# Performance work log

Hardware: AMD Instinct MI355X
Metric: run time of the kernel (lower is better)

Reference implementation:

```python
import jax, jax.numpy as jnp
import numpy as np

B, S, E, H = 32, 4096, 1024, 16
D = E // H  # head_dim = 64


def setup_inputs() -> dict:
    key = jax.random.key(0)
    ks = jax.random.split(key, 6)
    scale = 1.0 / np.sqrt(E)
    x = jax.random.normal(ks[0], (B, S, E), dtype=jnp.float32)
    mask = jax.random.randint(ks[1], (B, S), 0, 2).astype(bool)  # True = masked key
    in_proj_w = jax.random.uniform(ks[2], (3 * E, E), jnp.float32, -scale, scale)
    in_proj_b = jnp.zeros((3 * E,), jnp.float32)
    out_w = jax.random.uniform(ks[3], (E, E), jnp.float32, -scale, scale)
    out_b = jnp.zeros((E,), jnp.float32)
    return {"x": x, "mask": mask, "in_proj_w": in_proj_w, "in_proj_b": in_proj_b,
            "out_w": out_w, "out_b": out_b}


def reference(x, mask, in_proj_w, in_proj_b, out_w, out_b):
    # nn.MultiheadAttention with q = x[:, 0:1, :], k = v = x, key_padding_mask=mask
    Wq, Wk, Wv = in_proj_w[:E], in_proj_w[E:2 * E], in_proj_w[2 * E:]
    bq, bk, bv = in_proj_b[:E], in_proj_b[E:2 * E], in_proj_b[2 * E:]
    q = (x[:, 0, :] @ Wq.T + bq).reshape(B, H, D)            # (B,H,D)
    k = (x @ Wk.T + bk).reshape(B, S, H, D)                  # (B,S,H,D)
    v = (x @ Wv.T + bv).reshape(B, S, H, D)
    scores = jnp.einsum('bhd,bshd->bhs', q, k) / np.sqrt(D)  # (B,H,S)
    scores = jnp.where(mask[:, None, :], jnp.float32(-1e30), scores)
    attn = jax.nn.softmax(scores, axis=-1)                   # (B,H,S)
    ctx = jnp.einsum('bhs,bshd->bhd', attn, v).reshape(B, E)
    out = ctx @ out_w.T + out_b                              # (B,E) == attn_output.squeeze(1)
    attn_weights = attn.mean(axis=1)[:, None, :]             # (B,1,S): heads averaged
    return out, attn_weights
```

## Files before the change

kernel.cpp:

```cpp
#include <hip/hip_runtime.h>
#include <math.h>


constexpr int cB = 32, cS = 4096, cE = 1024, cH = 16, cD = 64, cNC = 16;

constexpr size_t OFF_P    = 0;
constexpr size_t OFF_C    = OFF_P + 524288;
constexpr size_t OFF_Q    = OFF_C + 512;
constexpr size_t OFF_SC   = OFF_Q + 32768;
constexpr size_t OFF_SM   = OFF_SC + 2097152;
constexpr size_t OFF_SL   = OFF_SM + 8192;
constexpr size_t OFF_MF   = OFF_SL + 8192;
constexpr size_t OFF_IL   = OFF_MF + 512;
constexpr size_t OFF_CTX  = OFF_IL + 512;
constexpr size_t OFF_PART = OFF_CTX + 32768;

__device__ inline float wave_max64(float v) {
#pragma unroll
  for (int m = 1; m < 64; m <<= 1) v = fmaxf(v, __shfl_xor(v, m));
  return v;
}
__device__ inline float wave_sum64(float v) {
#pragma unroll
  for (int m = 1; m < 64; m <<= 1) v += __shfl_xor(v, m);
  return v;
}

__global__ __launch_bounds__(256) void k1a_q(const float* __restrict__ x,
                                             const float* __restrict__ w,
                                             const float* __restrict__ bias,
                                             float* __restrict__ q) {
  int b = blockIdx.x >> 3, blk = blockIdx.x & 7;
  int tid = threadIdx.x;
  __shared__ float x0[cE];
  ((float4*)x0)[tid] = ((const float4*)(x + (size_t)b * cS * cE))[tid];
  __syncthreads();
  int row = blk * 128 + (tid >> 1);
  int half = tid & 1;
  const float* wr = w + (size_t)row * cE + half * 512;
  const float* xl = x0 + half * 512;
  float acc = 0.f;
#pragma unroll 4
  for (int j = 0; j < 128; ++j) {
    float4 a = *(const float4*)(wr + j * 4);
    float4 xv = *(const float4*)(xl + j * 4);
    acc = fmaf(a.x, xv.x, acc); acc = fmaf(a.y, xv.y, acc);
    acc = fmaf(a.z, xv.z, acc); acc = fmaf(a.w, xv.w, acc);
  }
  float tot = acc + __shfl_xor(acc, 1);
  if (!half) q[b * cE + row] = tot + bias[row];
}

__global__ __launch_bounds__(256) void k1b_p(const float* __restrict__ w,
                                             const float* __restrict__ bvec,
                                             const float* __restrict__ q,
                                             float* __restrict__ p,
                                             float* __restrict__ cb) {
  int b = blockIdx.x >> 3, sub = blockIdx.x & 7;
  int ec = sub >> 1, hh = sub & 1;
  int tid = threadIdx.x;
  int e = ec * 256 + tid;
  __shared__ float ql[cE];
  ((float4*)ql)[tid] = ((const float4*)(q + (size_t)b * cE))[tid];
  __syncthreads();
  for (int hi = 0; hi < 8; ++hi) {
    int h = hh * 8 + hi;
    float acc = 0.f;
    const float* wb = w + (size_t)(cE + h * cD) * cE + e;
    const float* qh = ql + h * cD;
#pragma unroll 8
    for (int d = 0; d < cD; ++d) acc = fmaf(wb[(size_t)d * cE], qh[d], acc);
    p[(size_t)(b * cH + h) * cE + e] = 0.125f * acc;
  }
  if (ec == 0 && tid < 8) {
    int h = hh * 8 + tid;
    float cacc = 0.f;
    for (int d = 0; d < cD; ++d) cacc = fmaf(ql[h * cD + d], bvec[cE + h * cD + d], cacc);
    cb[b * cH + h] = 0.125f * cacc;
  }
}

__global__ __launch_bounds__(256) void kfuse2(const float* __restrict__ x,
                                              const float* __restrict__ p,
                                              const float* __restrict__ cbias,
                                              const int* __restrict__ mask,
                                              float* __restrict__ scores,
                                              float* __restrict__ statsM,
                                              float* __restrict__ statsL,
                                              float* __restrict__ part) {
  __shared__ __align__(16) float smem[16384];
  int bx = blockIdx.x;
  int b = bx >> 4, sc = bx & 15;
  int s_base = sc * 256;
  int tid = threadIdx.x;
  int s_t = tid & 63, h_t = tid >> 6;
  int h0 = __builtin_amdgcn_readfirstlane(h_t * 4);
  float acc[4][4];
#pragma unroll
  for (int i = 0; i < 4; ++i)
#pragma unroll
    for (int j = 0; j < 4; ++j) acc[i][j] = 0.f;

  const float* xb = x + ((size_t)b * cS + s_base) * cE;
  const float* __restrict__ pu = p + (size_t)(b * cH + h0) * cE;

  float4 sv[8];
  int r_ = tid >> 3, c4_ = tid & 7;

#pragma unroll
  for (int i = 0; i < 8; ++i)
    sv[i] = *(const float4*)(xb + (size_t)(i * 32 + r_) * cE + c4_ * 4);
  {
    float* xd = smem;
#pragma unroll
    for (int i = 0; i < 8; ++i) {
      int r = i * 32 + r_;
      float vv[4] = {sv[i].x, sv[i].y, sv[i].z, sv[i].w};
#pragma unroll
      for (int j = 0; j < 4; ++j) {
        int e = c4_ * 4 + j;
        int f = (e ^ (e >> 4)) & 15;
        xd[e * 256 + ((((r >> 2) ^ f) << 2) | (r & 3))] = vv[j];
      }
    }
  }
  __syncthreads();

  for (int kt = 1; kt <= 32; ++kt) {
    if (kt < 32) {
#pragma unroll
      for (int i = 0; i < 8; ++i)
        sv[i] = *(const float4*)(xb + (size_t)(i * 32 + r_) * cE + kt * 32 + c4_ * 4);
    }
    {
      const float* xs = smem + ((kt - 1) & 1) * 8192;
      const int kb = (kt - 1) * 32;
#pragma unroll 8
      for (int e = 0; e < 32; ++e) {
        int f = (e ^ (e >> 4)) & 15;
        float4 xv = *(const float4*)&xs[e * 256 + ((s_t ^ f) << 2)];
        float p0 = pu[kb + e];
        float p1 = pu[cE + kb + e];
        float p2 = pu[2 * cE + kb + e];
        float p3 = pu[3 * cE + kb + e];
        float xa[4] = {xv.x, xv.y, xv.z, xv.w};
        float pa[4] = {p0, p1, p2, p3};
#pragma unroll
        for (int si = 0; si < 4; ++si)
#pragma unroll
          for (int hj = 0; hj < 4; ++hj) acc[si][hj] = fmaf(xa[si], pa[hj], acc[si][hj]);
      }
    }
    if (kt < 32) {
      float* xd = smem + (kt & 1) * 8192;
#pragma unroll
      for (int i = 0; i < 8; ++i) {
        int r = i * 32 + r_;
        float vv[4] = {sv[i].x, sv[i].y, sv[i].z, sv[i].w};
#pragma unroll
        for (int j = 0; j < 4; ++j) {
          int e = c4_ * 4 + j;
          int f = (e ^ (e >> 4)) & 15;
          xd[e * 256 + ((((r >> 2) ^ f) << 2) | (r & 3))] = vv[j];
        }
      }
    }
    __syncthreads();
  }

  float* al = smem;
  float4 cv = *(const float4*)(cbias + b * cH + h0);
  float ca[4] = {cv.x, cv.y, cv.z, cv.w};
  int4 m4 = *(const int4*)(mask + (size_t)b * cS + s_base + s_t * 4);
#pragma unroll
  for (int hj = 0; hj < 4; ++hj) {
    float v0 = m4.x ? -1e30f : acc[0][hj] + ca[hj];
    float v1 = m4.y ? -1e30f : acc[1][hj] + ca[hj];
    float v2 = m4.z ? -1e30f : acc[2][hj] + ca[hj];
    float v3 = m4.w ? -1e30f : acc[3][hj] + ca[hj];
    *(float4*)(scores + (size_t)(b * cH + h0 + hj) * cS + s_base + s_t * 4) =
        make_float4(v0, v1, v2, v3);
    float mx = fmaxf(fmaxf(v0, v1), fmaxf(v2, v3));
    float wm = wave_max64(mx);
    float e0 = __expf(v0 - wm), e1 = __expf(v1 - wm);
    float e2 = __expf(v2 - wm), e3 = __expf(v3 - wm);
    float wsum = wave_sum64(e0 + e1 + e2 + e3);
    if (s_t == 0) {
      statsM[(size_t)(b * cH + h0 + hj) * cNC + sc] = wm;
      statsL[(size_t)(b * cH + h0 + hj) * cNC + sc] = wsum;
    }
    int sl = s_t * 4;
    al[(sl + 0) * 20 + h0 + hj] = e0;
    al[(sl + 1) * 20 + h0 + hj] = e1;
    al[(sl + 2) * 20 + h0 + hj] = e2;
    al[(sl + 3) * 20 + h0 + hj] = e3;
  }
  __syncthreads();

  float4 acc2[16];
#pragma unroll
  for (int h = 0; h < cH; ++h) acc2[h] = make_float4(0.f, 0.f, 0.f, 0.f);
  const float* xg = xb + (size_t)tid * 4;
#pragma unroll 4
  for (int s = 0; s < 256; ++s) {
    float4 xv = *(const float4*)(xg + (size_t)s * cE);
    const float4* ar = (const float4*)(al + s * 20);
    float4 a0 = ar[0], a1 = ar[1], a2 = ar[2], a3 = ar[3];
    float aa[16] = {a0.x, a0.y, a0.z, a0.w, a1.x, a1.y, a1.z, a1.w,
                    a2.x, a2.y, a2.z, a2.w, a3.x, a3.y, a3.z, a3.w};
#pragma unroll
    for (int h = 0; h < cH; ++h) {
      acc2[h].x = fmaf(aa[h], xv.x, acc2[h].x);
      acc2[h].y = fmaf(aa[h], xv.y, acc2[h].y);
      acc2[h].z = fmaf(aa[h], xv.z, acc2[h].z);
      acc2[h].w = fmaf(aa[h], xv.w, acc2[h].w);
    }
  }
  float* pb = part + ((size_t)(b * cNC + sc) * cH) * cE + (size_t)tid * 4;
#pragma unroll
  for (int h = 0; h < cH; ++h) *(float4*)(pb + (size_t)h * cE) = acc2[h];
}

__global__ __launch_bounds__(256) void k5_ctx(const float* __restrict__ w,
                                              const float* __restrict__ bvec,
                                              const float* __restrict__ part,
                                              const float* __restrict__ statsM,
                                              const float* __restrict__ statsL,
                                              float* __restrict__ ctx,
                                              float* __restrict__ Mf,
                                              float* __restrict__ iLf) {
  int b = blockIdx.x >> 4, h = blockIdx.x & 15;
  int bh = b * cH + h;
  int tid = threadIdx.x;
  __shared__ float yl[cE];
  float M = -3e38f;
#pragma unroll
  for (int c = 0; c < cNC; ++c) M = fmaxf(M, statsM[bh * cNC + c]);
  float L = 0.f;
  float wgt[cNC];
#pragma unroll
  for (int c = 0; c < cNC; ++c) {
    wgt[c] = __expf(statsM[bh * cNC + c] - M);
    L += statsL[bh * cNC + c] * wgt[c];
  }
  float iL = 1.0f / L;
  if (tid == 0) { Mf[bh] = M; iLf[bh] = iL; }
  float4 a = make_float4(0.f, 0.f, 0.f, 0.f);
  const float* pb = part + (size_t)b * cNC * cH * cE + (size_t)h * cE + (size_t)tid * 4;
#pragma unroll
  for (int c = 0; c < cNC; ++c) {
    float4 v = *(const float4*)(pb + (size_t)c * cH * cE);
    a.x = fmaf(v.x, wgt[c], a.x); a.y = fmaf(v.y, wgt[c], a.y);
    a.z = fmaf(v.z, wgt[c], a.z); a.w = fmaf(v.w, wgt[c], a.w);
  }
  a.x *= iL; a.y *= iL; a.z *= iL; a.w *= iL;
  *(float4*)(yl + tid * 4) = a;
  __syncthreads();
  int wid = tid >> 6, lane = tid & 63;
  for (int i = 0; i < 16; ++i) {
    int d = wid * 16 + i;
    const float* wr = w + (size_t)(2 * cE + h * cD + d) * cE + lane * 16;
    const float* yr = yl + lane * 16;
    float partial = 0.f;
#pragma unroll
    for (int j = 0; j < 4; ++j) {
      float4 wv = *(const float4*)(wr + j * 4);
      float4 yv = *(const float4*)(yr + j * 4);
      partial = fmaf(wv.x, yv.x, partial); partial = fmaf(wv.y, yv.y, partial);
      partial = fmaf(wv.z, yv.z, partial); partial = fmaf(wv.w, yv.w, partial);
    }
    partial = wave_sum64(partial);
    if (lane == 0) ctx[b * cE + h * cD + d] = partial + bvec[2 * cE + h * cD + d];
  }
}

__global__ __launch_bounds__(256) void kmean(const float* __restrict__ scores,
                                             const float* __restrict__ Mf,
                                             const float* __restrict__ iLf,
                                             float* __restrict__ out) {
  int idx = blockIdx.x * 256 + threadIdx.x;
  int b = idx >> 12, s = idx & 4095;
  float sum = 0.f;
#pragma unroll
  for (int h = 0; h < cH; ++h) {
    float v = scores[(size_t)(b * cH + h) * cS + s];
    sum += __expf(v - Mf[b * cH + h]) * iLf[b * cH + h];
  }
  out[cB * cE + (size_t)b * cS + s] = sum * (1.0f / 16.0f);
}

__global__ __launch_bounds__(256) void k6_out(const float* __restrict__ w,
                                              const float* __restrict__ bvec,
                                              const float* __restrict__ ctx,
                                              float* __restrict__ out) {
  int b = blockIdx.x >> 3, br = blockIdx.x & 7;
  int tid = threadIdx.x;
  __shared__ float cl[cE];
  ((float4*)cl)[tid] = ((const float4*)(ctx + (size_t)b * cE))[tid];
  __syncthreads();
  int wid = tid >> 6, lane = tid & 63;
  for (int i = 0; i < 32; ++i) {
    int row = br * 128 + wid * 32 + i;
    const float* wr = w + (size_t)row * cE + lane * 16;
    const float* cr = cl + lane * 16;
    float partial = 0.f;
#pragma unroll
    for (int j = 0; j < 4; ++j) {
      float4 wv = *(const float4*)(wr + j * 4);
      float4 cv = *(const float4*)(cr + j * 4);
      partial = fmaf(wv.x, cv.x, partial); partial = fmaf(wv.y, cv.y, partial);
      partial = fmaf(wv.z, cv.z, partial); partial = fmaf(wv.w, cv.w, partial);
    }
    partial = wave_sum64(partial);
    if (lane == 0) out[(size_t)b * cE + row] = partial + bvec[row];
  }
}

extern "C" void kernel_launch(void* const* d_in, const int* in_sizes, int n_in,
                              void* d_out, int out_size, void* d_ws, size_t ws_size,
                              hipStream_t stream) {
  const float* x = (const float*)d_in[0];
  const int* mask = (const int*)d_in[1];
  const float* in_proj_w = (const float*)d_in[2];
  const float* in_proj_b = (const float*)d_in[3];
  const float* out_w = (const float*)d_in[4];
  const float* out_b = (const float*)d_in[5];
  float* out = (float*)d_out;
  float* W = (float*)d_ws;

  float* p = W + OFF_P;
  float* cb = W + OFF_C;
  float* q = W + OFF_Q;
  float* scores = W + OFF_SC;
  float* statsM = W + OFF_SM;
  float* statsL = W + OFF_SL;
  float* Mf = W + OFF_MF;
  float* iLf = W + OFF_IL;
  float* ctx = W + OFF_CTX;
  float* part = W + OFF_PART;

  k1a_q<<<256, 256, 0, stream>>>(x, in_proj_w, in_proj_b, q);
  k1b_p<<<256, 256, 0, stream>>>(in_proj_w, in_proj_b, q, p, cb);
  kfuse2<<<512, 256, 0, stream>>>(x, p, cb, mask, scores, statsM, statsL, part);
  k5_ctx<<<512, 256, 0, stream>>>(in_proj_w, in_proj_b, part, statsM, statsL, ctx, Mf, iLf);
  kmean<<<512, 256, 0, stream>>>(scores, Mf, iLf, out);
  k6_out<<<256, 256, 0, stream>>>(out_w, out_b, ctx, out);
}
```

Baseline: 345.2 us.

## Batch small projections into shared GEMM kernel and retile score computation

Replaces the per-batch matrix-vector kernels for the q, V and output projections with one reusable kernel, kgemm32. Each block of it stages all 32 batch rows in LDS, so every weight row is read once for the whole batch instead of once per batch element. The q·Wk product becomes a blocked kernel that tiles Wk and q through LDS. The score loop in kfuse2 is retiled to 2 positions by 8 heads per thread, which needs a cross-wave combination of softmax statistics through shared memory. The context combine now writes an intermediate y buffer to the workspace for the batched V projection, adding global traffic and a dependency.

```diff
diff --git a/kernel.cpp b/kernel.cpp
--- a/kernel.cpp
+++ b/kernel.cpp
@@ -14,6 +14,7 @@
 constexpr size_t OFF_IL   = OFF_MF + 512;
 constexpr size_t OFF_CTX  = OFF_IL + 512;
 constexpr size_t OFF_PART = OFF_CTX + 32768;
+constexpr size_t OFF_Y    = OFF_PART + 8388608;
 
 __device__ inline float wave_max64(float v) {
 #pragma unroll
@@ -26,57 +27,115 @@
   return v;
 }
 
-__global__ __launch_bounds__(256) void k1a_q(const float* __restrict__ x,
-                                             const float* __restrict__ w,
-                                             const float* __restrict__ bias,
-                                             float* __restrict__ q) {
-  int b = blockIdx.x >> 3, blk = blockIdx.x & 7;
+__global__ __launch_bounds__(256) void kgemm32(const float* __restrict__ A,
+                                               size_t aRowStride, int aBlk,
+                                               const float* __restrict__ Wm, int wRow0,
+                                               const float* __restrict__ bias,
+                                               float* __restrict__ C) {
+  __shared__ float a_lds[32 * 1028];
+  __shared__ float red[4][16][32];
   int tid = threadIdx.x;
-  __shared__ float x0[cE];
-  ((float4*)x0)[tid] = ((const float4*)(x + (size_t)b * cS * cE))[tid];
-  __syncthreads();
-  int row = blk * 128 + (tid >> 1);
-  int half = tid & 1;
-  const float* wr = w + (size_t)row * cE + half * 512;
-  const float* xl = x0 + half * 512;
-  float acc = 0.f;
-#pragma unroll 4
-  for (int j = 0; j < 128; ++j) {
-    float4 a = *(const float4*)(wr + j * 4);
-    float4 xv = *(const float4*)(xl + j * 4);
-    acc = fmaf(a.x, xv.x, acc); acc = fmaf(a.y, xv.y, acc);
-    acc = fmaf(a.z, xv.z, acc); acc = fmaf(a.w, xv.w, acc);
-  }
-  float tot = acc + __shfl_xor(acc, 1);
-  if (!half) q[b * cE + row] = tot + bias[row];
-}
-
-__global__ __launch_bounds__(256) void k1b_p(const float* __restrict__ w,
-                                             const float* __restrict__ bvec,
-                                             const float* __restrict__ q,
-                                             float* __restrict__ p,
-                                             float* __restrict__ cb) {
-  int b = blockIdx.x >> 3, sub = blockIdx.x & 7;
-  int ec = sub >> 1, hh = sub & 1;
+  int bx = blockIdx.x;
+  const float* abase = A + (aBlk ? ((size_t)(bx >> 2) * 1024) : (size_t)0);
+
+#pragma unroll 4
+  for (int j = 0; j < 32; ++j) {
+    float4 v = *(const float4*)(abase + (size_t)j * aRowStride + (size_t)tid * 4);
+    *(float4*)(a_lds + j * 1028 + tid * 4) = v;
+  }
+  __syncthreads();
+
+  int wv = tid >> 6, lane = tid & 63;
+  int ng = lane >> 4, bp = lane & 15;
+  float acc[4][2];
+#pragma unroll
+  for (int j = 0; j < 4; ++j) { acc[j][0] = 0.f; acc[j][1] = 0.f; }
+
+  const float* w0 = Wm + (size_t)(wRow0 + bx * 16 + ng * 4) * 1024;
+#pragma unroll 4
+  for (int i = 0; i < 64; ++i) {
+    int e4 = wv * 64 + ((i + bp) & 63);
+    float4 a0 = *(const float4*)(a_lds + (bp * 2 + 0) * 1028 + e4 * 4);
+    float4 a1 = *(const float4*)(a_lds + (bp * 2 + 1) * 1028 + e4 * 4);
+#pragma unroll
+    for (int j = 0; j < 4; ++j) {
+      float4 w4 = *(const float4*)(w0 + (size_t)j * 1024 + e4 * 4);
+      acc[j][0] = fmaf(w4.x, a0.x, acc[j][0]); acc[j][0] = fmaf(w4.y, a0.y, acc[j][0]);
+      acc[j][0] = fmaf(w4.z, a0.z, acc[j][0]); acc[j][0] = fmaf(w4.w, a0.w, acc[j][0]);
+      acc[j][1] = fmaf(w4.x, a1.x, acc[j][1]); acc[j][1] = fmaf(w4.y, a1.y, acc[j][1]);
+      acc[j][1] = fmaf(w4.z, a1.z, acc[j][1]); acc[j][1] = fmaf(w4.w, a1.w, acc[j][1]);
+    }
+  }
+#pragma unroll
+  for (int j = 0; j < 4; ++j) {
+    red[wv][ng * 4 + j][bp * 2 + 0] = acc[j][0];
+    red[wv][ng * 4 + j][bp * 2 + 1] = acc[j][1];
+  }
+  __syncthreads();
+#pragma unroll
+  for (int t = 0; t < 2; ++t) {
+    int idx = t * 256 + tid;
+    int n = idx >> 5, b = idx & 31;
+    float s = red[0][n][b] + red[1][n][b] + red[2][n][b] + red[3][n][b] +
+              bias[bx * 16 + n];
+    C[(size_t)b * 1024 + bx * 16 + n] = s;
+  }
+}
+
+__global__ __launch_bounds__(256) void kp_gemm(const float* __restrict__ w,
+                                               const float* __restrict__ bvec,
+                                               const float* __restrict__ q,
+                                               float* __restrict__ p,
+                                               float* __restrict__ cb) {
+  __shared__ float w_lds[64 * 260];
+  __shared__ float q_lds[32 * 65];
+  int h = blockIdx.x >> 2, et = blockIdx.x & 3;
   int tid = threadIdx.x;
-  int e = ec * 256 + tid;
-  __shared__ float ql[cE];
-  ((float4*)ql)[tid] = ((const float4*)(q + (size_t)b * cE))[tid];
-  __syncthreads();
-  for (int hi = 0; hi < 8; ++hi) {
-    int h = hh * 8 + hi;
-    float acc = 0.f;
-    const float* wb = w + (size_t)(cE + h * cD) * cE + e;
-    const float* qh = ql + h * cD;
-#pragma unroll 8
-    for (int d = 0; d < cD; ++d) acc = fmaf(wb[(size_t)d * cE], qh[d], acc);
-    p[(size_t)(b * cH + h) * cE + e] = 0.125f * acc;
-  }
-  if (ec == 0 && tid < 8) {
-    int h = hh * 8 + tid;
+#pragma unroll 4
+  for (int j = 0; j < 16; ++j) {
+    int idx = j * 256 + tid;
+    int row = idx >> 6, c4 = idx & 63;
+    float4 v = *(const float4*)(w + (size_t)(1024 + h * 64 + row) * 1024 + et * 256 + c4 * 4);
+    *(float4*)(w_lds + row * 260 + c4 * 4) = v;
+  }
+#pragma unroll
+  for (int jj = 0; jj < 2; ++jj) {
+    int idx = jj * 256 + tid;
+    int row = idx >> 4, c4 = idx & 15;
+    float4 v = *(const float4*)(q + (size_t)row * 1024 + h * 64 + c4 * 4);
+    *(float4*)(q_lds + row * 65 + c4 * 4) = v;
+  }
+  __syncthreads();
+
+  int b = tid & 31, eg = tid >> 5;
+  float4 acc[8];
+#pragma unroll
+  for (int j = 0; j < 8; ++j) acc[j] = make_float4(0.f, 0.f, 0.f, 0.f);
+#pragma unroll 4
+  for (int d = 0; d < 64; ++d) {
+    float qv = q_lds[b * 65 + d];
+#pragma unroll
+    for (int j = 0; j < 8; ++j) {
+      float4 wv4 = *(const float4*)(w_lds + d * 260 + eg * 32 + j * 4);
+      acc[j].x = fmaf(wv4.x, qv, acc[j].x);
+      acc[j].y = fmaf(wv4.y, qv, acc[j].y);
+      acc[j].z = fmaf(wv4.z, qv, acc[j].z);
+      acc[j].w = fmaf(wv4.w, qv, acc[j].w);
+    }
+  }
+  float* pb = p + (size_t)(b * cH + h) * cE + et * 256 + eg * 32;
+#pragma unroll
+  for (int j = 0; j < 8; ++j) {
+    float4 o = make_float4(acc[j].x * 0.125f, acc[j].y * 0.125f,
+                           acc[j].z * 0.125f, acc[j].w * 0.125f);
+    *(float4*)(pb + j * 4) = o;
+  }
+  if (et == 0 && tid < 32) {
+    int bb = tid;
     float cacc = 0.f;
-    for (int d = 0; d < cD; ++d) cacc = fmaf(ql[h * cD + d], bvec[cE + h * cD + d], cacc);
-    cb[b * cH + h] = 0.125f * cacc;
+    for (int d = 0; d < 64; ++d)
+      cacc = fmaf(q_lds[bb * 65 + d], bvec[1024 + h * 64 + d], cacc);
+    cb[bb * cH + h] = 0.125f * cacc;
   }
 }
 
@@ -89,17 +148,19 @@
                                               float* __restrict__ statsL,
                                               float* __restrict__ part) {
   __shared__ __align__(16) float smem[16384];
+  __shared__ float sml_m[4][8], sml_l[4][8];
   int bx = blockIdx.x;
   int b = bx >> 4, sc = bx & 15;
   int s_base = sc * 256;
   int tid = threadIdx.x;
-  int s_t = tid & 63, h_t = tid >> 6;
-  int h0 = __builtin_amdgcn_readfirstlane(h_t * 4);
-  float acc[4][4];
-#pragma unroll
-  for (int i = 0; i < 4; ++i)
-#pragma unroll
-    for (int j = 0; j < 4; ++j) acc[i][j] = 0.f;
+  int wv = tid >> 6, lane = tid & 63;
+  int sg = wv & 1, hg = wv >> 1;
+  int h0 = __builtin_amdgcn_readfirstlane(hg * 8);
+  float acc[2][8];
+#pragma unroll
+  for (int i = 0; i < 2; ++i)
+#pragma unroll
+    for (int j = 0; j < 8; ++j) acc[i][j] = 0.f;
 
   const float* xb = x + ((size_t)b * cS + s_base) * cE;
   const float* __restrict__ pu = p + (size_t)(b * cH + h0) * cE;
@@ -126,6 +187,8 @@
   }
   __syncthreads();
 
+  int gbase = sg * 32 + (lane >> 1);
+  int goff = (lane & 1) << 1;
   for (int kt = 1; kt <= 32; ++kt) {
     if (kt < 32) {
 #pragma unroll
@@ -138,17 +201,21 @@
 #pragma unroll 8
       for (int e = 0; e < 32; ++e) {
         int f = (e ^ (e >> 4)) & 15;
-        float4 xv = *(const float4*)&xs[e * 256 + ((s_t ^ f) << 2)];
+        float2 xv = *(const float2*)&xs[e * 256 + (((gbase ^ f) << 2) | goff)];
         float p0 = pu[kb + e];
         float p1 = pu[cE + kb + e];
         float p2 = pu[2 * cE + kb + e];
         float p3 = pu[3 * cE + kb + e];
-        float xa[4] = {xv.x, xv.y, xv.z, xv.w};
-        float pa[4] = {p0, p1, p2, p3};
-#pragma unroll
-        for (int si = 0; si < 4; ++si)
-#pragma unroll
-          for (int hj = 0; hj < 4; ++hj) acc[si][hj] = fmaf(xa[si], pa[hj], acc[si][hj]);
+        float p4 = pu[4 * cE + kb + e];
+        float p5 = pu[5 * cE + kb + e];
+        float p6 = pu[6 * cE + kb + e];
+        float p7 = pu[7 * cE + kb + e];
+        float pa[8] = {p0, p1, p2, p3, p4, p5, p6, p7};
+#pragma unroll
+        for (int hj = 0; hj < 8; ++hj) {
+          acc[0][hj] = fmaf(xv.x, pa[hj], acc[0][hj]);
+          acc[1][hj] = fmaf(xv.y, pa[hj], acc[1][hj]);
+        }
       }
     }
     if (kt < 32) {
@@ -169,40 +236,53 @@
   }
 
   float* al = smem;
-  float4 cv = *(const float4*)(cbias + b * cH + h0);
-  float ca[4] = {cv.x, cv.y, cv.z, cv.w};
-  int4 m4 = *(const int4*)(mask + (size_t)b * cS + s_base + s_t * 4);
-#pragma unroll
-  for (int hj = 0; hj < 4; ++hj) {
-    float v0 = m4.x ? -1e30f : acc[0][hj] + ca[hj];
-    float v1 = m4.y ? -1e30f : acc[1][hj] + ca[hj];
-    float v2 = m4.z ? -1e30f : acc[2][hj] + ca[hj];
-    float v3 = m4.w ? -1e30f : acc[3][hj] + ca[hj];
-    *(float4*)(scores + (size_t)(b * cH + h0 + hj) * cS + s_base + s_t * 4) =
-        make_float4(v0, v1, v2, v3);
-    float mx = fmaxf(fmaxf(v0, v1), fmaxf(v2, v3));
-    float wm = wave_max64(mx);
-    float e0 = __expf(v0 - wm), e1 = __expf(v1 - wm);
-    float e2 = __expf(v2 - wm), e3 = __expf(v3 - wm);
-    float wsum = wave_sum64(e0 + e1 + e2 + e3);
-    if (s_t == 0) {
-      statsM[(size_t)(b * cH + h0 + hj) * cNC + sc] = wm;
-      statsL[(size_t)(b * cH + h0 + hj) * cNC + sc] = wsum;
-    }
-    int sl = s_t * 4;
-    al[(sl + 0) * 20 + h0 + hj] = e0;
-    al[(sl + 1) * 20 + h0 + hj] = e1;
-    al[(sl + 2) * 20 + h0 + hj] = e2;
-    al[(sl + 3) * 20 + h0 + hj] = e3;
-  }
-  __syncthreads();
+  int sl_loc = sg * 128 + lane * 2;
+  int sl = s_base + sl_loc;
+  float ca[8];
+  {
+    float4 c0 = *(const float4*)(cbias + b * cH + h0);
+    float4 c1 = *(const float4*)(cbias + b * cH + h0 + 4);
+    ca[0] = c0.x; ca[1] = c0.y; ca[2] = c0.z; ca[3] = c0.w;
+    ca[4] = c1.x; ca[5] = c1.y; ca[6] = c1.z; ca[7] = c1.w;
+  }
+  int2 mv = *(const int2*)(mask + (size_t)b * cS + sl);
+  float vs0[8], vs1[8];
+#pragma unroll
+  for (int hj = 0; hj < 8; ++hj) {
+    float v0 = mv.x ? -1e30f : acc[0][hj] + ca[hj];
+    float v1 = mv.y ? -1e30f : acc[1][hj] + ca[hj];
+    vs0[hj] = v0; vs1[hj] = v1;
+    float2 o = make_float2(v0, v1);
+    *(float2*)(scores + (size_t)(b * cH + h0 + hj) * cS + sl) = o;
+    float wm = wave_max64(fmaxf(v0, v1));
+    if (lane == 0) sml_m[wv][hj] = wm;
+  }
+  __syncthreads();
+#pragma unroll
+  for (int hj = 0; hj < 8; ++hj) {
+    float mh = fmaxf(sml_m[hg * 2][hj], sml_m[hg * 2 + 1][hj]);
+    float e0 = __expf(vs0[hj] - mh);
+    float e1 = __expf(vs1[hj] - mh);
+    float ws = wave_sum64(e0 + e1);
+    if (lane == 0) sml_l[wv][hj] = ws;
+    al[(sl_loc + 0) * 20 + h0 + hj] = e0;
+    al[(sl_loc + 1) * 20 + h0 + hj] = e1;
+  }
+  __syncthreads();
+  if (tid < 16) {
+    int h = tid, hg2 = h >> 3, hj = h & 7;
+    float mh = fmaxf(sml_m[hg2 * 2][hj], sml_m[hg2 * 2 + 1][hj]);
+    float L = sml_l[hg2 * 2][hj] + sml_l[hg2 * 2 + 1][hj];
+    statsM[(size_t)(b * cH + h) * cNC + sc] = mh;
+    statsL[(size_t)(b * cH + h) * cNC + sc] = L;
+  }
 
   float4 acc2[16];
 #pragma unroll
   for (int h = 0; h < cH; ++h) acc2[h] = make_float4(0.f, 0.f, 0.f, 0.f);
   const float* xg = xb + (size_t)tid * 4;
 #pragma unroll 4
-  for (int s = 0; s < 256; ++s) {
+  for (int s = 255; s >= 0; --s) {
     float4 xv = *(const float4*)(xg + (size_t)s * cE);
     const float4* ar = (const float4*)(al + s * 20);
     float4 a0 = ar[0], a1 = ar[1], a2 = ar[2], a3 = ar[3];
@@ -221,18 +301,15 @@
   for (int h = 0; h < cH; ++h) *(float4*)(pb + (size_t)h * cE) = acc2[h];
 }
 
-__global__ __launch_bounds__(256) void k5_ctx(const float* __restrict__ w,
-                                              const float* __restrict__ bvec,
-                                              const float* __restrict__ part,
-                                              const float* __restrict__ statsM,
-                                              const float* __restrict__ statsL,
-                                              float* __restrict__ ctx,
-                                              float* __restrict__ Mf,
-                                              float* __restrict__ iLf) {
+__global__ __launch_bounds__(256) void k5a_comb(const float* __restrict__ part,
+                                                const float* __restrict__ statsM,
+                                                const float* __restrict__ statsL,
+                                                float* __restrict__ y,
+                                                float* __restrict__ Mf,
+                                                float* __restrict__ iLf) {
   int b = blockIdx.x >> 4, h = blockIdx.x & 15;
   int bh = b * cH + h;
   int tid = threadIdx.x;
-  __shared__ float yl[cE];
   float M = -3e38f;
 #pragma unroll
   for (int c = 0; c < cNC; ++c) M = fmaxf(M, statsM[bh * cNC + c]);
@@ -254,24 +331,7 @@
     a.z = fmaf(v.z, wgt[c], a.z); a.w = fmaf(v.w, wgt[c], a.w);
   }
   a.x *= iL; a.y *= iL; a.z *= iL; a.w *= iL;
-  *(float4*)(yl + tid * 4) = a;
-  __syncthreads();
-  int wid = tid >> 6, lane = tid & 63;
-  for (int i = 0; i < 16; ++i) {
-    int d = wid * 16 + i;
-    const float* wr = w + (size_t)(2 * cE + h * cD + d) * cE + lane * 16;
-    const float* yr = yl + lane * 16;
-    float partial = 0.f;
-#pragma unroll
-    for (int j = 0; j < 4; ++j) {
-      float4 wv = *(const float4*)(wr + j * 4);
-      float4 yv = *(const float4*)(yr + j * 4);
-      partial = fmaf(wv.x, yv.x, partial); partial = fmaf(wv.y, yv.y, partial);
-      partial = fmaf(wv.z, yv.z, partial); partial = fmaf(wv.w, yv.w, partial);
-    }
-    partial = wave_sum64(partial);
-    if (lane == 0) ctx[b * cE + h * cD + d] = partial + bvec[2 * cE + h * cD + d];
-  }
+  *(float4*)(y + (size_t)bh * cE + (size_t)tid * 4) = a;
 }
 
 __global__ __launch_bounds__(256) void kmean(const float* __restrict__ scores,
@@ -287,33 +347,6 @@
     sum += __expf(v - Mf[b * cH + h]) * iLf[b * cH + h];
   }
   out[cB * cE + (size_t)b * cS + s] = sum * (1.0f / 16.0f);
-}
-
-__global__ __launch_bounds__(256) void k6_out(const float* __restrict__ w,
-                                              const float* __restrict__ bvec,
-                                              const float* __restrict__ ctx,
-                                              float* __restrict__ out) {
-  int b = blockIdx.x >> 3, br = blockIdx.x & 7;
-  int tid = threadIdx.x;
-  __shared__ float cl[cE];
-  ((float4*)cl)[tid] = ((const float4*)(ctx + (size_t)b * cE))[tid];
-  __syncthreads();
-  int wid = tid >> 6, lane = tid & 63;
-  for (int i = 0; i < 32; ++i) {
-    int row = br * 128 + wid * 32 + i;
-    const float* wr = w + (size_t)row * cE + lane * 16;
-    const float* cr = cl + lane * 16;
-    float partial = 0.f;
-#pragma unroll
-    for (int j = 0; j < 4; ++j) {
-      float4 wv = *(const float4*)(wr + j * 4);
-      float4 cv = *(const float4*)(cr + j * 4);
-      partial = fmaf(wv.x, cv.x, partial); partial = fmaf(wv.y, cv.y, partial);
-      partial = fmaf(wv.z, cv.z, partial); partial = fmaf(wv.w, cv.w, partial);
-    }
-    partial = wave_sum64(partial);
-    if (lane == 0) out[(size_t)b * cE + row] = partial + bvec[row];
-  }
 }
 
 extern "C" void kernel_launch(void* const* d_in, const int* in_sizes, int n_in,
@@ -338,11 +371,14 @@
   float* iLf = W + OFF_IL;
   float* ctx = W + OFF_CTX;
   float* part = W + OFF_PART;
-
-  k1a_q<<<256, 256, 0, stream>>>(x, in_proj_w, in_proj_b, q);
-  k1b_p<<<256, 256, 0, stream>>>(in_proj_w, in_proj_b, q, p, cb);
+  float* y = W + OFF_Y;
+
+  kgemm32<<<64, 256, 0, stream>>>(x, (size_t)cS * cE, 0, in_proj_w, 0, in_proj_b, q);
+  kp_gemm<<<64, 256, 0, stream>>>(in_proj_w, in_proj_b, q, p, cb);
   kfuse2<<<512, 256, 0, stream>>>(x, p, cb, mask, scores, statsM, statsL, part);
-  k5_ctx<<<512, 256, 0, stream>>>(in_proj_w, in_proj_b, part, statsM, statsL, ctx, Mf, iLf);
+  k5a_comb<<<512, 256, 0, stream>>>(part, statsM, statsL, y, Mf, iLf);
+  kgemm32<<<64, 256, 0, stream>>>(y, (size_t)cH * cE, 1, in_proj_w, 2048,
+                                  in_proj_b + 2048, ctx);
   kmean<<<512, 256, 0, stream>>>(scores, Mf, iLf, out);
-  k6_out<<<256, 256, 0, stream>>>(out_w, out_b, ctx, out);
-}
+  kgemm32<<<64, 256, 0, stream>>>(ctx, (size_t)cE, 0, out_w, 0, out_b, out);
+}
```

Measured after the change: 300.7 us, median of 2. -12.9%, faster.
